# Kernel optimization log

Hardware: AMD Instinct MI355X
Metric: run time of the kernel (lower is better)

Reference implementation:

```python
import jax, jax.numpy as jnp
import numpy as np

D = 288
H = 8
HD = D // H  # 36
LAYER_TYPES = ['attn' if i % 3 == 0 else 'rec' for i in range(1, 15)]  # 4 attn, 10 rec


def rmsnorm(x, scale, eps=1e-6):
    # matches torch: ||x||_2 / sqrt(d), then scale * x / (norm + eps)
    norm = jnp.linalg.norm(x, axis=-1, keepdims=True) * (x.shape[-1] ** -0.5)
    return scale * x / (norm + eps)


def attention(x, w_qkv, w_out, nscale):
    B, L, Dm = x.shape
    r = x
    x = rmsnorm(x, nscale)
    qkv = x @ w_qkv.T  # [B,L,3D]
    q, k, v = jnp.split(qkv, 3, axis=-1)
    sh = lambda t: t.reshape(B, L, H, HD).transpose(0, 2, 1, 3)  # [B,H,L,hd]
    q, k, v = sh(q), sh(k), sh(v)
    scores = jnp.einsum('bhqd,bhkd->bhqk', q, k) / jnp.sqrt(jnp.float32(HD))
    mask = jnp.tril(jnp.ones((L, L), dtype=bool))
    scores = jnp.where(mask, scores, -jnp.inf)
    p = jax.nn.softmax(scores, axis=-1)
    o = jnp.einsum('bhqk,bhkd->bhqd', p, v).transpose(0, 2, 1, 3).reshape(B, L, Dm)
    return r + o @ w_out.T


def recurrence(x, w_in, w_out, nscale):
    r = x
    x = rmsnorm(x, nscale)
    gvf = x @ w_in.T  # [B,L,3D]
    g, v, f = jnp.split(gvf, 3, axis=-1)
    g = jax.nn.sigmoid(g)
    f = jax.nn.sigmoid(f - 1.0)
    B, L, Dm = v.shape

    def step(h, fv):
        ft, vt = fv
        h = ft * h + (1.0 - ft) * vt
        return h, h

    _, hs = jax.lax.scan(step, jnp.zeros((B, Dm), v.dtype),
                         (f.transpose(1, 0, 2), v.transpose(1, 0, 2)))
    h_seq = hs.transpose(1, 0, 2)  # [B,L,D]
    return r + (g * h_seq) @ w_out.T


def ffn(x, wg, wu, wd, nscale):
    r = x
    x = rmsnorm(x, nscale)
    return r + (jax.nn.silu(x @ wg.T) * (x @ wu.T)) @ wd.T


def setup_inputs() -> dict:
    key = jax.random.key(0)
    ks = jax.random.split(key, 16)
    n = lambda k, shape, std=0.02: jax.random.normal(k, shape, jnp.float32) * std
    return dict(
        x=jax.random.randint(ks[0], (32, 512), 0, 4096),
        emb=n(ks[1], (4096, 288)),
        pos_emb=n(ks[2], (512, 288), 0.01),
        attn_qkv=n(ks[3], (4, 864, 288)),
        attn_out=n(ks[4], (4, 288, 288)),
        attn_norm=jnp.ones((4, 288), jnp.float32),
        rec_in=n(ks[5], (10, 864, 288)),
        rec_out=n(ks[6], (10, 288, 288)),
        rec_norm=jnp.ones((10, 288), jnp.float32),
        ffn_gate=n(ks[7], (14, 864, 288)),
        ffn_up=n(ks[8], (14, 864, 288)),
        ffn_down=n(ks[9], (14, 288, 864)),
        ffn_norm=jnp.ones((14, 288), jnp.float32),
        final_norm=jnp.ones((288,), jnp.float32),
    )


def reference(x, emb, pos_emb, attn_qkv, attn_out, attn_norm,
              rec_in, rec_out, rec_norm,
              ffn_gate, ffn_up, ffn_down, ffn_norm, final_norm):
    L = x.shape[1]
    h = emb[x] + pos_emb[jnp.arange(L)]
    ai = ri = 0
    for i, t in enumerate(LAYER_TYPES):
        if t == 'attn':
            h = attention(h, attn_qkv[ai], attn_out[ai], attn_norm[ai])
            ai += 1
        else:
            h = recurrence(h, rec_in[ri], rec_out[ri], rec_norm[ri])
            ri += 1
        h = ffn(h, ffn_gate[i], ffn_up[i], ffn_down[i], ffn_norm[i])
    h = rmsnorm(h, final_norm)
    return h @ emb.T  # [B,L,V] tied-embedding logits
```

## Files before the change

kernel.cpp:

```cpp
#include <hip/hip_runtime.h>
#include <hip/hip_bf16.h>
#include <math.h>
#include <stdint.h>

using bf16 = __hip_bfloat16;
typedef __attribute__((ext_vector_type(8))) short short8;
typedef __attribute__((ext_vector_type(4))) float f32x4;

#define LOG2E 1.44269504088896340736f

enum { EPI_BF16 = 0, EPI_GVF = 1, EPI_F32 = 3 };

__device__ __forceinline__ float bf2f(bf16 v) { return __bfloat162float(v); }
__device__ __forceinline__ bf16 f2bf(float v) { return __float2bfloat16(v); }
__device__ __forceinline__ unsigned short f2bfraw(float f) {
  bf16 h = __float2bfloat16(f);
  unsigned short u;
  __builtin_memcpy(&u, &h, 2);
  return u;
}
__device__ __forceinline__ float braw2f(unsigned short u) {
  unsigned x = (unsigned)u << 16;
  float f;
  __builtin_memcpy(&f, &x, 4);
  return f;
}

__device__ __forceinline__ int swz64(int row, int col) {
  return row * 32 + ((((col >> 3) ^ ((row >> 1) & 3)) << 3) | (col & 7));
}
__device__ __forceinline__ int swz128(int row, int col) {
  return row * 64 + ((((col >> 3) ^ (row & 7)) << 3) | (col & 7));
}

__device__ __forceinline__ void gload16(const bf16* src, bf16* dst) {
  __builtin_amdgcn_global_load_lds(
      (const __attribute__((address_space(1))) void*)src,
      (__attribute__((address_space(3))) void*)dst, 16, 0, 0);
}

__global__ void cvt_kernel(const float* __restrict__ in, bf16* __restrict__ out, int n4) {
  int i = blockIdx.x * 256 + threadIdx.x;
  if (i >= n4) return;
  const float4 v = ((const float4*)in)[i];
  uint2 pk;
  pk.x = (unsigned)f2bfraw(v.x) | ((unsigned)f2bfraw(v.y) << 16);
  pk.y = (unsigned)f2bfraw(v.z) | ((unsigned)f2bfraw(v.w) << 16);
  ((uint2*)out)[i] = pk;
}

__global__ __launch_bounds__(256) void embed_norm_kernel(const int* __restrict__ x,
                                                         const float* __restrict__ emb,
                                                         const float* __restrict__ pos,
                                                         const float* __restrict__ sc,
                                                         float* __restrict__ hbuf,
                                                         bf16* __restrict__ xn) {
  int row = blockIdx.x * 4 + (threadIdx.x >> 6);
  int lane = threadIdx.x & 63;
  int tok = x[row];
  const float* e = emb + (size_t)tok * 288;
  const float* p = pos + (size_t)(row & 511) * 288;
  float v[5];
  float ss = 0.f;
#pragma unroll
  for (int j = 0; j < 4; ++j) {
    v[j] = e[j * 64 + lane] + p[j * 64 + lane];
    ss += v[j] * v[j];
  }
  v[4] = (lane < 32) ? (e[256 + lane] + p[256 + lane]) : 0.f;
  ss += v[4] * v[4];
#pragma unroll
  for (int off = 32; off > 0; off >>= 1) ss += __shfl_xor(ss, off);
  float inv = 1.f / (sqrtf(ss * (1.f / 288.f)) + 1e-6f);
  float* hr = hbuf + (size_t)row * 288;
  bf16* xr = xn + (size_t)row * 288;
#pragma unroll
  for (int j = 0; j < 4; ++j) {
    hr[j * 64 + lane] = v[j];
    xr[j * 64 + lane] = f2bf(v[j] * inv * sc[j * 64 + lane]);
  }
  if (lane < 32) {
    hr[256 + lane] = v[4];
    xr[256 + lane] = f2bf(v[4] * inv * sc[256 + lane]);
  }
}

__global__ __launch_bounds__(64) void scanA_kernel(const bf16* __restrict__ gvf,
                                                   float* __restrict__ Ap,
                                                   float* __restrict__ Bp) {
  int g = blockIdx.x * 64 + threadIdx.x;
  int c = blockIdx.y;
  int b = g / 144, dp = g - b * 144;
  const bf16* base = gvf + (size_t)b * 512 * 864 + (size_t)c * 32 * 864 + dp * 2;
  float A0 = 1.f, A1 = 1.f, B0 = 0.f, B1 = 0.f;
#pragma unroll 4
  for (int t = 0; t < 32; ++t) {
    unsigned vv = *(const unsigned*)(base + (size_t)t * 864 + 288);
    unsigned ff = *(const unsigned*)(base + (size_t)t * 864 + 576);
    float v0 = braw2f((unsigned short)vv), v1 = braw2f((unsigned short)(vv >> 16));
    float f0 = braw2f((unsigned short)ff), f1 = braw2f((unsigned short)(ff >> 16));
    B0 = f0 * B0 + (1.f - f0) * v0;
    B1 = f1 * B1 + (1.f - f1) * v1;
    A0 *= f0;
    A1 *= f1;
  }
  int half = b * 144 + dp;
  ((float2*)(Ap + (size_t)c * 9216))[half] = make_float2(A0, A1);
  ((float2*)(Bp + (size_t)c * 9216))[half] = make_float2(B0, B1);
}

__global__ __launch_bounds__(64) void scanC_kernel(const bf16* __restrict__ gvf,
                                                   const float* __restrict__ Ap,
                                                   const float* __restrict__ Bp,
                                                   bf16* __restrict__ y) {
  int g = blockIdx.x * 64 + threadIdx.x;
  int c = blockIdx.y;
  int b = g / 144, dp = g - b * 144;
  int half = b * 144 + dp;
  float h0 = 0.f, h1 = 0.f;
  for (int cc = 0; cc < c; ++cc) {
    float2 a = ((const float2*)(Ap + (size_t)cc * 9216))[half];
    float2 bb = ((const float2*)(Bp + (size_t)cc * 9216))[half];
    h0 = bb.x + a.x * h0;
    h1 = bb.y + a.y * h1;
  }
  const bf16* base = gvf + (size_t)b * 512 * 864 + (size_t)c * 32 * 864 + dp * 2;
  bf16* yb = y + (size_t)b * 512 * 288 + (size_t)c * 32 * 288 + dp * 2;
#pragma unroll 4
  for (int t = 0; t < 32; ++t) {
    unsigned gg = *(const unsigned*)(base + (size_t)t * 864);
    unsigned vv = *(const unsigned*)(base + (size_t)t * 864 + 288);
    unsigned ff = *(const unsigned*)(base + (size_t)t * 864 + 576);
    float g0 = braw2f((unsigned short)gg), g1 = braw2f((unsigned short)(gg >> 16));
    float v0 = braw2f((unsigned short)vv), v1 = braw2f((unsigned short)(vv >> 16));
    float f0 = braw2f((unsigned short)ff), f1 = braw2f((unsigned short)(ff >> 16));
    h0 = f0 * h0 + (1.f - f0) * v0;
    h1 = f1 * h1 + (1.f - f1) * v1;
    unsigned o = (unsigned)f2bfraw(g0 * h0) | ((unsigned)f2bfraw(g1 * h1) << 16);
    *(unsigned*)(yb + (size_t)t * 288) = o;
  }
}

template <int BN, int EPI>
__global__ __launch_bounds__(256) void gemm_kernel(const bf16* __restrict__ A,
                                                   const bf16* __restrict__ W,
                                                   void* __restrict__ outv,
                                                   int N, int K) {
  constexpr int WN = BN / 2;
  constexpr int NF = WN / 16;
  constexpr int TC = 8 + BN / 16;
  __shared__ __align__(16) bf16 As[2][128 * 32];
  __shared__ __align__(16) bf16 Bs[2][BN * 32];
  const int tid = threadIdx.x;
  const int w = tid >> 6, l = tid & 63;
  const int m0 = blockIdx.x * 128;
  const int n0 = blockIdx.y * BN;
  const int nk = K >> 5;
  const int lrow = l >> 2, lslot = l & 3;

  auto stage = [&](int buf, int kt) {
    for (int wc = w; wc < TC; wc += 4) {
      const bf16* src;
      bf16* dst;
      int row;
      if (wc < 8) {
        row = wc * 16 + lrow;
        src = A + (size_t)(m0 + row) * K;
        dst = &As[buf][wc * 512];
      } else {
        row = (wc - 8) * 16 + lrow;
        src = W + (size_t)(n0 + row) * K;
        dst = &Bs[buf][(wc - 8) * 512];
      }
      int slot = lslot ^ ((row >> 1) & 3);
      gload16(src + kt * 32 + slot * 8, dst);
    }
  };

  f32x4 acc[4][NF];
#pragma unroll
  for (int a = 0; a < 4; ++a)
#pragma unroll
    for (int b = 0; b < NF; ++b) acc[a][b] = (f32x4){0.f, 0.f, 0.f, 0.f};

  stage(0, 0);
  __syncthreads();
  for (int kt = 0; kt < nk; ++kt) {
    int cur = kt & 1;
    if (kt + 1 < nk) stage(cur ^ 1, kt + 1);
    short8 af[4], bfr[NF];
#pragma unroll
    for (int mf = 0; mf < 4; ++mf)
      af[mf] = *(const short8*)&As[cur][swz64((w >> 1) * 64 + mf * 16 + (l & 15), (l >> 4) * 8)];
#pragma unroll
    for (int nf = 0; nf < NF; ++nf)
      bfr[nf] = *(const short8*)&Bs[cur][swz64((w & 1) * WN + nf * 16 + (l & 15), (l >> 4) * 8)];
#pragma unroll
    for (int mf = 0; mf < 4; ++mf)
#pragma unroll
      for (int nf = 0; nf < NF; ++nf)
        acc[mf][nf] = __builtin_amdgcn_mfma_f32_16x16x32_bf16(af[mf], bfr[nf], acc[mf][nf], 0, 0, 0);
    __syncthreads();
  }

#pragma unroll
  for (int mf = 0; mf < 4; ++mf) {
#pragma unroll
    for (int nf = 0; nf < NF; ++nf) {
#pragma unroll
      for (int rr = 0; rr < 4; ++rr) {
        int row = m0 + (w >> 1) * 64 + mf * 16 + (l >> 4) * 4 + rr;
        int col = n0 + (w & 1) * WN + nf * 16 + (l & 15);
        float v = acc[mf][nf][rr];
        size_t o = (size_t)row * N + col;
        if (EPI == EPI_BF16) {
          ((bf16*)outv)[o] = f2bf(v);
        } else if (EPI == EPI_GVF) {
          float z;
          if (col < 288) z = 1.f / (1.f + __expf(-v));
          else if (col < 576) z = v;
          else z = 1.f / (1.f + __expf(-(v - 1.f)));
          ((bf16*)outv)[o] = f2bf(z);
        } else {
          ((float*)outv)[o] = v;
        }
      }
    }
  }
}

__global__ __launch_bounds__(256) void gemm_row_kernel(const bf16* __restrict__ A,
                                                       const bf16* __restrict__ W,
                                                       float* __restrict__ hbuf,
                                                       bf16* __restrict__ xn,
                                                       const float* __restrict__ scale,
                                                       int K) {
  __shared__ __align__(16) bf16 As[2][64 * 32];
  __shared__ __align__(16) bf16 Bs[2][288 * 32];
  __shared__ float ssx[2][64];
  const int tid = threadIdx.x;
  const int w = tid >> 6, l = tid & 63;
  const int m0 = blockIdx.x * 64;
  const int nk = K >> 5;
  const int lrow = l >> 2, lslot = l & 3;

  auto stage = [&](int buf, int kt) {
    for (int wc = w; wc < 22; wc += 4) {
      const bf16* src;
      bf16* dst;
      int row;
      if (wc < 4) {
        row = wc * 16 + lrow;
        src = A + (size_t)(m0 + row) * K;
        dst = &As[buf][wc * 512];
      } else {
        row = (wc - 4) * 16 + lrow;
        src = W + (size_t)row * K;
        dst = &Bs[buf][(wc - 4) * 512];
      }
      int slot = lslot ^ ((row >> 1) & 3);
      gload16(src + kt * 32 + slot * 8, dst);
    }
  };

  f32x4 acc[2][9];
#pragma unroll
  for (int a = 0; a < 2; ++a)
#pragma unroll
    for (int b = 0; b < 9; ++b) acc[a][b] = (f32x4){0.f, 0.f, 0.f, 0.f};

  stage(0, 0);
  __syncthreads();
  for (int kt = 0; kt < nk; ++kt) {
    int cur = kt & 1;
    if (kt + 1 < nk) stage(cur ^ 1, kt + 1);
    short8 af[2];
#pragma unroll
    for (int mf = 0; mf < 2; ++mf)
      af[mf] = *(const short8*)&As[cur][swz64((w >> 1) * 32 + mf * 16 + (l & 15), (l >> 4) * 8)];
#pragma unroll
    for (int nf = 0; nf < 9; ++nf) {
      short8 bv = *(const short8*)&Bs[cur][swz64((w & 1) * 144 + nf * 16 + (l & 15), (l >> 4) * 8)];
      acc[0][nf] = __builtin_amdgcn_mfma_f32_16x16x32_bf16(af[0], bv, acc[0][nf], 0, 0, 0);
      acc[1][nf] = __builtin_amdgcn_mfma_f32_16x16x32_bf16(af[1], bv, acc[1][nf], 0, 0, 0);
    }
    __syncthreads();
  }

  float ss[2][4];
#pragma unroll
  for (int mf = 0; mf < 2; ++mf)
#pragma unroll
    for (int rr = 0; rr < 4; ++rr) ss[mf][rr] = 0.f;

#pragma unroll
  for (int mf = 0; mf < 2; ++mf)
#pragma unroll
    for (int nf = 0; nf < 9; ++nf)
#pragma unroll
      for (int rr = 0; rr < 4; ++rr) {
        int rowl = (w >> 1) * 32 + mf * 16 + (l >> 4) * 4 + rr;
        int col = (w & 1) * 144 + nf * 16 + (l & 15);
        size_t o = (size_t)(m0 + rowl) * 288 + col;
        float v = acc[mf][nf][rr] + hbuf[o];
        hbuf[o] = v;
        acc[mf][nf][rr] = v;
        ss[mf][rr] += v * v;
      }
#pragma unroll
  for (int off = 1; off < 16; off <<= 1)
#pragma unroll
    for (int mf = 0; mf < 2; ++mf)
#pragma unroll
      for (int rr = 0; rr < 4; ++rr) ss[mf][rr] += __shfl_xor(ss[mf][rr], off);
  if ((l & 15) == 0) {
#pragma unroll
    for (int mf = 0; mf < 2; ++mf)
#pragma unroll
      for (int rr = 0; rr < 4; ++rr)
        ssx[w & 1][(w >> 1) * 32 + mf * 16 + (l >> 4) * 4 + rr] = ss[mf][rr];
  }
  __syncthreads();
  float inv[2][4];
#pragma unroll
  for (int mf = 0; mf < 2; ++mf)
#pragma unroll
    for (int rr = 0; rr < 4; ++rr) {
      int rowl = (w >> 1) * 32 + mf * 16 + (l >> 4) * 4 + rr;
      float tot = ssx[0][rowl] + ssx[1][rowl];
      inv[mf][rr] = 1.f / (sqrtf(tot * (1.f / 288.f)) + 1e-6f);
    }
#pragma unroll
  for (int nf = 0; nf < 9; ++nf) {
    int col = (w & 1) * 144 + nf * 16 + (l & 15);
    float sc = scale[col];
#pragma unroll
    for (int mf = 0; mf < 2; ++mf)
#pragma unroll
      for (int rr = 0; rr < 4; ++rr) {
        int rowl = (w >> 1) * 32 + mf * 16 + (l >> 4) * 4 + rr;
        size_t o = (size_t)(m0 + rowl) * 288 + col;
        xn[o] = f2bf(acc[mf][nf][rr] * inv[mf][rr] * sc);
      }
  }
}

__global__ __launch_bounds__(256) void gateup_kernel(const bf16* __restrict__ A,
                                                     const bf16* __restrict__ Wg,
                                                     const bf16* __restrict__ Wu,
                                                     bf16* __restrict__ out, int N, int K) {
  constexpr int WN = 48, NF = 3;
  __shared__ __align__(16) bf16 As[2][128 * 32];
  __shared__ __align__(16) bf16 Bg[2][96 * 32];
  __shared__ __align__(16) bf16 Bu[2][96 * 32];
  const int tid = threadIdx.x;
  const int w = tid >> 6, l = tid & 63;
  const int m0 = blockIdx.x * 128;
  const int n0 = blockIdx.y * 96;
  const int nk = K >> 5;
  const int lrow = l >> 2, lslot = l & 3;

  auto stage = [&](int buf, int kt) {
    for (int wc = w; wc < 20; wc += 4) {
      const bf16* src;
      bf16* dst;
      int row;
      if (wc < 8) {
        row = wc * 16 + lrow;
        src = A + (size_t)(m0 + row) * K;
        dst = &As[buf][wc * 512];
      } else if (wc < 14) {
        row = (wc - 8) * 16 + lrow;
        src = Wg + (size_t)(n0 + row) * K;
        dst = &Bg[buf][(wc - 8) * 512];
      } else {
        row = (wc - 14) * 16 + lrow;
        src = Wu + (size_t)(n0 + row) * K;
        dst = &Bu[buf][(wc - 14) * 512];
      }
      int slot = lslot ^ ((row >> 1) & 3);
      gload16(src + kt * 32 + slot * 8, dst);
    }
  };

  f32x4 accg[4][NF], accu[4][NF];
#pragma unroll
  for (int a = 0; a < 4; ++a)
#pragma unroll
    for (int b = 0; b < NF; ++b) {
      accg[a][b] = (f32x4){0.f, 0.f, 0.f, 0.f};
      accu[a][b] = (f32x4){0.f, 0.f, 0.f, 0.f};
    }

  stage(0, 0);
  __syncthreads();
  for (int kt = 0; kt < nk; ++kt) {
    int cur = kt & 1;
    if (kt + 1 < nk) stage(cur ^ 1, kt + 1);
    short8 af[4], bg[NF], bu[NF];
#pragma unroll
    for (int mf = 0; mf < 4; ++mf)
      af[mf] = *(const short8*)&As[cur][swz64((w >> 1) * 64 + mf * 16 + (l & 15), (l >> 4) * 8)];
#pragma unroll
    for (int nf = 0; nf < NF; ++nf) {
      bg[nf] = *(const short8*)&Bg[cur][swz64((w & 1) * WN + nf * 16 + (l & 15), (l >> 4) * 8)];
      bu[nf] = *(const short8*)&Bu[cur][swz64((w & 1) * WN + nf * 16 + (l & 15), (l >> 4) * 8)];
    }
#pragma unroll
    for (int mf = 0; mf < 4; ++mf)
#pragma unroll
      for (int nf = 0; nf < NF; ++nf) {
        accg[mf][nf] = __builtin_amdgcn_mfma_f32_16x16x32_bf16(af[mf], bg[nf], accg[mf][nf], 0, 0, 0);
        accu[mf][nf] = __builtin_amdgcn_mfma_f32_16x16x32_bf16(af[mf], bu[nf], accu[mf][nf], 0, 0, 0);
      }
    __syncthreads();
  }

#pragma unroll
  for (int mf = 0; mf < 4; ++mf)
#pragma unroll
    for (int nf = 0; nf < NF; ++nf)
#pragma unroll
      for (int rr = 0; rr < 4; ++rr) {
        int row = m0 + (w >> 1) * 64 + mf * 16 + (l >> 4) * 4 + rr;
        int col = n0 + (w & 1) * WN + nf * 16 + (l & 15);
        float g = accg[mf][nf][rr], u = accu[mf][nf][rr];
        float s = g / (1.f + __expf(-g));
        out[(size_t)row * N + col] = f2bf(s * u);
      }
}

__global__ __launch_bounds__(256) void attn_kernel(const bf16* __restrict__ qkv,
                                                   bf16* __restrict__ y) {
  const int bid = blockIdx.x;
  const int qb = bid & 7, hh = (bid >> 3) & 7, b = bid >> 6;
  const int tid = threadIdx.x, w = tid >> 6, l = tid & 63;
  __shared__ __align__(16) bf16 Qs[64 * 64];
  __shared__ __align__(16) bf16 Ks[64 * 64];
  __shared__ __align__(16) bf16 Vt[48 * 64];
  __shared__ __align__(16) bf16 Ps[64 * 64];
  const size_t bbase = (size_t)b * 512 * 864;

  for (int idx = tid; idx < 64 * 64; idx += 256) {
    ((unsigned short*)Qs)[idx] = 0;
    ((unsigned short*)Ks)[idx] = 0;
  }
  for (int idx = tid; idx < 48 * 64; idx += 256) ((unsigned short*)Vt)[idx] = 0;

  const bf16* qp = qkv + bbase + (size_t)(qb * 64) * 864 + hh * 36;
  for (int idx = tid; idx < 64 * 36; idx += 256) {
    int row = idx / 36, c = idx - row * 36;
    Qs[swz128(row, c)] = qp[(size_t)row * 864 + c];
  }
  __syncthreads();

  f32x4 oacc[3];
#pragma unroll
  for (int f = 0; f < 3; ++f) oacc[f] = (f32x4){0.f, 0.f, 0.f, 0.f};
  float mprev[4] = {-1e30f, -1e30f, -1e30f, -1e30f};
  float lsum[4] = {0.f, 0.f, 0.f, 0.f};
  const int qrow_base = qb * 64 + w * 16;

  for (int kt = 0; kt <= qb; ++kt) {
    const bf16* kp = qkv + bbase + (size_t)(kt * 64) * 864 + 288 + hh * 36;
    const bf16* vp = qkv + bbase + (size_t)(kt * 64) * 864 + 576 + hh * 36;
    for (int idx = tid; idx < 64 * 36; idx += 256) {
      int row = idx / 36, c = idx - row * 36;
      Ks[swz128(row, c)] = kp[(size_t)row * 864 + c];
      Vt[swz128(c, row)] = vp[(size_t)row * 864 + c];
    }
    __syncthreads();

    f32x4 sacc[4];
#pragma unroll
    for (int n = 0; n < 4; ++n) sacc[n] = (f32x4){0.f, 0.f, 0.f, 0.f};
#pragma unroll
    for (int s = 0; s < 2; ++s) {
      short8 aq = *(const short8*)&Qs[swz128(w * 16 + (l & 15), s * 32 + (l >> 4) * 8)];
#pragma unroll
      for (int n = 0; n < 4; ++n) {
        short8 bk = *(const short8*)&Ks[swz128(n * 16 + (l & 15), s * 32 + (l >> 4) * 8)];
        sacc[n] = __builtin_amdgcn_mfma_f32_16x16x32_bf16(aq, bk, sacc[n], 0, 0, 0);
      }
    }

    const bool diag = (kt == qb);
    float mt[4];
#pragma unroll
    for (int rr = 0; rr < 4; ++rr) {
      int qg = qrow_base + (l >> 4) * 4 + rr;
      float mx = -1e30f;
#pragma unroll
      for (int n = 0; n < 4; ++n) {
        float sv = sacc[n][rr] * (1.f / 6.f);
        if (diag) {
          int kg = kt * 64 + n * 16 + (l & 15);
          if (kg > qg) sv = -1e30f;
        }
        sacc[n][rr] = sv;
        mx = fmaxf(mx, sv);
      }
      mt[rr] = mx;
    }
#pragma unroll
    for (int off = 1; off < 16; off <<= 1)
#pragma unroll
      for (int rr = 0; rr < 4; ++rr) mt[rr] = fmaxf(mt[rr], __shfl_xor(mt[rr], off));

    float alpha[4], rs[4];
#pragma unroll
    for (int rr = 0; rr < 4; ++rr) {
      float mn = fmaxf(mprev[rr], mt[rr]);
      alpha[rr] = exp2f((mprev[rr] - mn) * LOG2E);
      mprev[rr] = mn;
      float ps = 0.f;
#pragma unroll
      for (int n = 0; n < 4; ++n) {
        float p = exp2f((sacc[n][rr] - mn) * LOG2E);
        sacc[n][rr] = p;
        ps += p;
      }
      rs[rr] = ps;
    }
#pragma unroll
    for (int off = 1; off < 16; off <<= 1)
#pragma unroll
      for (int rr = 0; rr < 4; ++rr) rs[rr] += __shfl_xor(rs[rr], off);
#pragma unroll
    for (int rr = 0; rr < 4; ++rr) lsum[rr] = lsum[rr] * alpha[rr] + rs[rr];
#pragma unroll
    for (int f = 0; f < 3; ++f)
#pragma unroll
      for (int rr = 0; rr < 4; ++rr) oacc[f][rr] *= alpha[rr];

#pragma unroll
    for (int n = 0; n < 4; ++n)
#pragma unroll
      for (int rr = 0; rr < 4; ++rr)
        Ps[swz128(w * 16 + (l >> 4) * 4 + rr, n * 16 + (l & 15))] = f2bf(sacc[n][rr]);
    __syncthreads();

#pragma unroll
    for (int s = 0; s < 2; ++s) {
      short8 ap = *(const short8*)&Ps[swz128(w * 16 + (l & 15), s * 32 + (l >> 4) * 8)];
#pragma unroll
      for (int f = 0; f < 3; ++f) {
        short8 bv = *(const short8*)&Vt[swz128(f * 16 + (l & 15), s * 32 + (l >> 4) * 8)];
        oacc[f] = __builtin_amdgcn_mfma_f32_16x16x32_bf16(ap, bv, oacc[f], 0, 0, 0);
      }
    }
    __syncthreads();
  }

#pragma unroll
  for (int rr = 0; rr < 4; ++rr) {
    float inv = 1.f / lsum[rr];
    int row = b * 512 + qb * 64 + w * 16 + (l >> 4) * 4 + rr;
    bf16* yr = y + (size_t)row * 288 + hh * 36;
#pragma unroll
    for (int f = 0; f < 3; ++f) {
      int col = f * 16 + (l & 15);
      if (col < 36) yr[col] = f2bf(oacc[f][rr] * inv);
    }
  }
}

extern "C" void kernel_launch(void* const* d_in, const int* in_sizes, int n_in,
                              void* d_out, int out_size, void* d_ws, size_t ws_size,
                              hipStream_t stream) {
  (void)in_sizes; (void)n_in; (void)out_size; (void)ws_size;
  const int* x = (const int*)d_in[0];
  const float* emb = (const float*)d_in[1];
  const float* pos = (const float*)d_in[2];
  const float* aqkv = (const float*)d_in[3];
  const float* aout = (const float*)d_in[4];
  const float* anorm = (const float*)d_in[5];
  const float* rin = (const float*)d_in[6];
  const float* rout = (const float*)d_in[7];
  const float* rnorm = (const float*)d_in[8];
  const float* fgate = (const float*)d_in[9];
  const float* fup = (const float*)d_in[10];
  const float* fdown = (const float*)d_in[11];
  const float* fnorm = (const float*)d_in[12];
  const float* finalnorm = (const float*)d_in[13];

  char* ws = (char*)d_ws;
  size_t off = 0;
  auto alloc = [&](size_t bytes) -> char* {
    char* p = ws + off;
    off += (bytes + 255) & ~(size_t)255;
    return p;
  };
  bf16* wqkv = (bf16*)alloc(4ull * 864 * 288 * 2);
  bf16* wao = (bf16*)alloc(4ull * 288 * 288 * 2);
  bf16* wrin = (bf16*)alloc(10ull * 864 * 288 * 2);
  bf16* wrout = (bf16*)alloc(10ull * 288 * 288 * 2);
  bf16* wg = (bf16*)alloc(14ull * 864 * 288 * 2);
  bf16* wu = (bf16*)alloc(14ull * 864 * 288 * 2);
  bf16* wd = (bf16*)alloc(14ull * 288 * 864 * 2);
  bf16* wemb = (bf16*)alloc(4096ull * 288 * 2);
  float* hbuf = (float*)alloc(16384ull * 288 * 4);
  bf16* xn = (bf16*)alloc(16384ull * 288 * 2);
  bf16* gvf = (bf16*)alloc(16384ull * 864 * 2);
  bf16* ybuf = (bf16*)alloc(16384ull * 288 * 2);
  float* Ap = (float*)alloc(16ull * 9216 * 4);
  float* Bp = (float*)alloc(16ull * 9216 * 4);

  auto cvt = [&](const float* src, bf16* dst, size_t n) {
    int n4 = (int)(n / 4);
    cvt_kernel<<<(n4 + 255) / 256, 256, 0, stream>>>(src, dst, n4);
  };
  cvt(aqkv, wqkv, 4ull * 864 * 288);
  cvt(aout, wao, 4ull * 288 * 288);
  cvt(rin, wrin, 10ull * 864 * 288);
  cvt(rout, wrout, 10ull * 288 * 288);
  cvt(fgate, wg, 14ull * 864 * 288);
  cvt(fup, wu, 14ull * 864 * 288);
  cvt(fdown, wd, 14ull * 288 * 864);
  cvt(emb, wemb, 4096ull * 288);

  const float* lnorm[15];
  {
    int a2 = 0, r2 = 0;
    for (int j = 0; j < 14; ++j) {
      if ((j + 1) % 3 == 0) lnorm[j] = anorm + (a2++) * 288;
      else lnorm[j] = rnorm + (r2++) * 288;
    }
    lnorm[14] = finalnorm;
  }

  embed_norm_kernel<<<4096, 256, 0, stream>>>(x, emb, pos, lnorm[0], hbuf, xn);

  int ai = 0, ri = 0;
  for (int i = 0; i < 14; ++i) {
    const bool isattn = ((i + 1) % 3 == 0);
    if (isattn) {
      gemm_kernel<96, EPI_BF16><<<dim3(128, 9), 256, 0, stream>>>(
          xn, wqkv + (size_t)ai * 864 * 288, gvf, 864, 288);
      attn_kernel<<<2048, 256, 0, stream>>>(gvf, ybuf);
      gemm_row_kernel<<<256, 256, 0, stream>>>(
          ybuf, wao + (size_t)ai * 288 * 288, hbuf, xn, fnorm + i * 288, 288);
      ++ai;
    } else {
      gemm_kernel<96, EPI_GVF><<<dim3(128, 9), 256, 0, stream>>>(
          xn, wrin + (size_t)ri * 864 * 288, gvf, 864, 288);
      scanA_kernel<<<dim3(72, 16), 64, 0, stream>>>(gvf, Ap, Bp);
      scanC_kernel<<<dim3(72, 16), 64, 0, stream>>>(gvf, Ap, Bp, ybuf);
      gemm_row_kernel<<<256, 256, 0, stream>>>(
          ybuf, wrout + (size_t)ri * 288 * 288, hbuf, xn, fnorm + i * 288, 288);
      ++ri;
    }
    gateup_kernel<<<dim3(128, 9), 256, 0, stream>>>(
        xn, wg + (size_t)i * 864 * 288, wu + (size_t)i * 864 * 288, gvf, 864, 288);
    gemm_row_kernel<<<256, 256, 0, stream>>>(
        gvf, wd + (size_t)i * 288 * 864, hbuf, xn, lnorm[i + 1], 864);
  }
  gemm_kernel<128, EPI_F32><<<dim3(128, 32), 256, 0, stream>>>(
      xn, wemb, d_out, 4096, 288);
}
```

Baseline: 2.646 ms.

## Fuse recurrence scan chunk-reduction into input GEMM, merge weight casts, widen row GEMM

The recurrence input GEMM now tiles output columns so that each block holds matching g, v and f channels. In its epilogue it computes the per-32-step chunk carry products (A, B) with lane shuffles, which removes the separate scanA pass that re-read gvf. The eight weight conversion launches become one kernel that selects source and destination by index range. The row-wise residual+norm GEMM goes to 512 threads, with each wave owning 16 rows, to raise occupancy. The trade-offs are a heavier GEMM epilogue with scattered stores, and fewer accumulators per wave in the row GEMM.

```diff
diff --git a/kernel.cpp b/kernel.cpp
--- a/kernel.cpp
+++ b/kernel.cpp
@@ -9,7 +9,7 @@
 
 #define LOG2E 1.44269504088896340736f
 
-enum { EPI_BF16 = 0, EPI_GVF = 1, EPI_F32 = 3 };
+enum { EPI_BF16 = 0, EPI_F32 = 3 };
 
 __device__ __forceinline__ float bf2f(bf16 v) { return __bfloat162float(v); }
 __device__ __forceinline__ bf16 f2bf(float v) { return __float2bfloat16(v); }
@@ -39,14 +39,28 @@
       (__attribute__((address_space(3))) void*)dst, 16, 0, 0);
 }
 
-__global__ void cvt_kernel(const float* __restrict__ in, bf16* __restrict__ out, int n4) {
+struct CvtPtrs {
+  const float* s[8];
+  bf16* d[8];
+};
+__global__ __launch_bounds__(256) void cvt_all_kernel(CvtPtrs p) {
   int i = blockIdx.x * 256 + threadIdx.x;
-  if (i >= n4) return;
-  const float4 v = ((const float4*)in)[i];
+  const float* src;
+  bf16* dst;
+  int li = i;
+  if (i < 248832)       { src = p.s[0]; dst = p.d[0]; }
+  else if (i < 331776)  { src = p.s[1]; dst = p.d[1]; li = i - 248832; }
+  else if (i < 953856)  { src = p.s[2]; dst = p.d[2]; li = i - 331776; }
+  else if (i < 1161216) { src = p.s[3]; dst = p.d[3]; li = i - 953856; }
+  else if (i < 2032128) { src = p.s[4]; dst = p.d[4]; li = i - 1161216; }
+  else if (i < 2903040) { src = p.s[5]; dst = p.d[5]; li = i - 2032128; }
+  else if (i < 3773952) { src = p.s[6]; dst = p.d[6]; li = i - 2903040; }
+  else                  { src = p.s[7]; dst = p.d[7]; li = i - 3773952; }
+  const float4 v = ((const float4*)src)[li];
   uint2 pk;
   pk.x = (unsigned)f2bfraw(v.x) | ((unsigned)f2bfraw(v.y) << 16);
   pk.y = (unsigned)f2bfraw(v.z) | ((unsigned)f2bfraw(v.w) << 16);
-  ((uint2*)out)[i] = pk;
+  ((uint2*)dst)[li] = pk;
 }
 
 __global__ __launch_bounds__(256) void embed_norm_kernel(const int* __restrict__ x,
@@ -83,30 +97,6 @@
     hr[256 + lane] = v[4];
     xr[256 + lane] = f2bf(v[4] * inv * sc[256 + lane]);
   }
-}
-
-__global__ __launch_bounds__(64) void scanA_kernel(const bf16* __restrict__ gvf,
-                                                   float* __restrict__ Ap,
-                                                   float* __restrict__ Bp) {
-  int g = blockIdx.x * 64 + threadIdx.x;
-  int c = blockIdx.y;
-  int b = g / 144, dp = g - b * 144;
-  const bf16* base = gvf + (size_t)b * 512 * 864 + (size_t)c * 32 * 864 + dp * 2;
-  float A0 = 1.f, A1 = 1.f, B0 = 0.f, B1 = 0.f;
-#pragma unroll 4
-  for (int t = 0; t < 32; ++t) {
-    unsigned vv = *(const unsigned*)(base + (size_t)t * 864 + 288);
-    unsigned ff = *(const unsigned*)(base + (size_t)t * 864 + 576);
-    float v0 = braw2f((unsigned short)vv), v1 = braw2f((unsigned short)(vv >> 16));
-    float f0 = braw2f((unsigned short)ff), f1 = braw2f((unsigned short)(ff >> 16));
-    B0 = f0 * B0 + (1.f - f0) * v0;
-    B1 = f1 * B1 + (1.f - f1) * v1;
-    A0 *= f0;
-    A1 *= f1;
-  }
-  int half = b * 144 + dp;
-  ((float2*)(Ap + (size_t)c * 9216))[half] = make_float2(A0, A1);
-  ((float2*)(Bp + (size_t)c * 9216))[half] = make_float2(B0, B1);
 }
 
 __global__ __launch_bounds__(64) void scanC_kernel(const bf16* __restrict__ gvf,
@@ -215,12 +205,6 @@
         size_t o = (size_t)row * N + col;
         if (EPI == EPI_BF16) {
           ((bf16*)outv)[o] = f2bf(v);
-        } else if (EPI == EPI_GVF) {
-          float z;
-          if (col < 288) z = 1.f / (1.f + __expf(-v));
-          else if (col < 576) z = v;
-          else z = 1.f / (1.f + __expf(-(v - 1.f)));
-          ((bf16*)outv)[o] = f2bf(z);
         } else {
           ((float*)outv)[o] = v;
         }
@@ -229,7 +213,125 @@
   }
 }
 
-__global__ __launch_bounds__(256) void gemm_row_kernel(const bf16* __restrict__ A,
+__global__ __launch_bounds__(256) void gemm_gvf_scan_kernel(const bf16* __restrict__ A,
+                                                            const bf16* __restrict__ W,
+                                                            bf16* __restrict__ gvf,
+                                                            float* __restrict__ Ap,
+                                                            float* __restrict__ Bp,
+                                                            int K) {
+  __shared__ __align__(16) bf16 As[2][128 * 32];
+  __shared__ __align__(16) bf16 Bs[2][96 * 32];
+  const int tid = threadIdx.x;
+  const int w = tid >> 6, l = tid & 63;
+  const int m0 = blockIdx.x * 128;
+  const int ch0 = blockIdx.y * 32;
+  const int nk = K >> 5;
+  const int lrow = l >> 2, lslot = l & 3;
+
+  auto stage = [&](int buf, int kt) {
+    for (int wc = w; wc < 14; wc += 4) {
+      const bf16* src;
+      bf16* dst;
+      int ldsrow;
+      if (wc < 8) {
+        ldsrow = wc * 16 + lrow;
+        src = A + (size_t)(m0 + ldsrow) * K;
+        dst = &As[buf][wc * 512];
+      } else {
+        int r96 = (wc - 8) * 16 + lrow;
+        ldsrow = r96;
+        int gr = r96 >> 4;
+        int sec = (gr >= 3) ? (gr - 3) : gr;
+        int offc = (gr >= 3) ? 16 : 0;
+        src = W + (size_t)(sec * 288 + ch0 + offc + (r96 & 15)) * K;
+        dst = &Bs[buf][(wc - 8) * 512];
+      }
+      int slot = lslot ^ ((ldsrow >> 1) & 3);
+      gload16(src + kt * 32 + slot * 8, dst);
+    }
+  };
+
+  f32x4 acc[4][3];
+#pragma unroll
+  for (int a = 0; a < 4; ++a)
+#pragma unroll
+    for (int b = 0; b < 3; ++b) acc[a][b] = (f32x4){0.f, 0.f, 0.f, 0.f};
+
+  stage(0, 0);
+  __syncthreads();
+  for (int kt = 0; kt < nk; ++kt) {
+    int cur = kt & 1;
+    if (kt + 1 < nk) stage(cur ^ 1, kt + 1);
+    short8 af[4], bfr[3];
+#pragma unroll
+    for (int mf = 0; mf < 4; ++mf)
+      af[mf] = *(const short8*)&As[cur][swz64((w >> 1) * 64 + mf * 16 + (l & 15), (l >> 4) * 8)];
+#pragma unroll
+    for (int nf = 0; nf < 3; ++nf)
+      bfr[nf] = *(const short8*)&Bs[cur][swz64((w & 1) * 48 + nf * 16 + (l & 15), (l >> 4) * 8)];
+#pragma unroll
+    for (int mf = 0; mf < 4; ++mf)
+#pragma unroll
+      for (int nf = 0; nf < 3; ++nf)
+        acc[mf][nf] = __builtin_amdgcn_mfma_f32_16x16x32_bf16(af[mf], bfr[nf], acc[mf][nf], 0, 0, 0);
+    __syncthreads();
+  }
+
+  const int chg = ch0 + (w & 1) * 16 + (l & 15);
+  const int bb = m0 >> 9;
+  const int lq = l >> 4;
+  float Asub[4], Bsub[4];
+#pragma unroll
+  for (int mf = 0; mf < 4; ++mf) {
+    float Aa = 1.f, Bb = 0.f;
+#pragma unroll
+    for (int rr = 0; rr < 4; ++rr) {
+      int row = m0 + (w >> 1) * 64 + mf * 16 + lq * 4 + rr;
+      float gv = acc[mf][0][rr];
+      float vv = acc[mf][1][rr];
+      float fv = acc[mf][2][rr];
+      float gs = 1.f / (1.f + __expf(-gv));
+      float fs = 1.f / (1.f + __expf(-(fv - 1.f)));
+      bf16 gb = f2bf(gs), vb = f2bf(vv), fb = f2bf(fs);
+      bf16* gp = gvf + (size_t)row * 864;
+      gp[chg] = gb;
+      gp[288 + chg] = vb;
+      gp[576 + chg] = fb;
+      float fr = bf2f(fb), vr = bf2f(vb);
+      Aa = fr * Aa;
+      Bb = fr * Bb + (1.f - fr) * vr;
+    }
+    Asub[mf] = Aa;
+    Bsub[mf] = Bb;
+  }
+#pragma unroll
+  for (int mf = 0; mf < 4; ++mf) {
+#pragma unroll
+    for (int bit = 16; bit <= 32; bit <<= 1) {
+      float Ao = __shfl_xor(Asub[mf], bit);
+      float Bo = __shfl_xor(Bsub[mf], bit);
+      if (l & bit) {
+        Bsub[mf] = Asub[mf] * Bo + Bsub[mf];
+        Asub[mf] = Asub[mf] * Ao;
+      } else {
+        Bsub[mf] = Ao * Bsub[mf] + Bo;
+        Asub[mf] = Ao * Asub[mf];
+      }
+    }
+  }
+  if (lq == 0) {
+    float Ac0 = Asub[1] * Asub[0], Bc0 = Asub[1] * Bsub[0] + Bsub[1];
+    float Ac1 = Asub[3] * Asub[2], Bc1 = Asub[3] * Bsub[2] + Bsub[3];
+    int cbase = ((m0 & 511) >> 5) + (w >> 1) * 2;
+    size_t ix = (size_t)bb * 288 + chg;
+    Ap[(size_t)cbase * 9216 + ix] = Ac0;
+    Bp[(size_t)cbase * 9216 + ix] = Bc0;
+    Ap[(size_t)(cbase + 1) * 9216 + ix] = Ac1;
+    Bp[(size_t)(cbase + 1) * 9216 + ix] = Bc1;
+  }
+}
+
+__global__ __launch_bounds__(512) void gemm_row_kernel(const bf16* __restrict__ A,
                                                        const bf16* __restrict__ W,
                                                        float* __restrict__ hbuf,
                                                        bf16* __restrict__ xn,
@@ -240,12 +342,13 @@
   __shared__ float ssx[2][64];
   const int tid = threadIdx.x;
   const int w = tid >> 6, l = tid & 63;
+  const int wm = w >> 1, wn = w & 1;
   const int m0 = blockIdx.x * 64;
   const int nk = K >> 5;
   const int lrow = l >> 2, lslot = l & 3;
 
   auto stage = [&](int buf, int kt) {
-    for (int wc = w; wc < 22; wc += 4) {
+    for (int wc = w; wc < 22; wc += 8) {
       const bf16* src;
       bf16* dst;
       int row;
@@ -263,85 +366,63 @@
     }
   };
 
-  f32x4 acc[2][9];
-#pragma unroll
-  for (int a = 0; a < 2; ++a)
-#pragma unroll
-    for (int b = 0; b < 9; ++b) acc[a][b] = (f32x4){0.f, 0.f, 0.f, 0.f};
+  f32x4 acc[9];
+#pragma unroll
+  for (int b = 0; b < 9; ++b) acc[b] = (f32x4){0.f, 0.f, 0.f, 0.f};
 
   stage(0, 0);
   __syncthreads();
   for (int kt = 0; kt < nk; ++kt) {
     int cur = kt & 1;
     if (kt + 1 < nk) stage(cur ^ 1, kt + 1);
-    short8 af[2];
-#pragma unroll
-    for (int mf = 0; mf < 2; ++mf)
-      af[mf] = *(const short8*)&As[cur][swz64((w >> 1) * 32 + mf * 16 + (l & 15), (l >> 4) * 8)];
+    short8 af = *(const short8*)&As[cur][swz64(wm * 16 + (l & 15), (l >> 4) * 8)];
 #pragma unroll
     for (int nf = 0; nf < 9; ++nf) {
-      short8 bv = *(const short8*)&Bs[cur][swz64((w & 1) * 144 + nf * 16 + (l & 15), (l >> 4) * 8)];
-      acc[0][nf] = __builtin_amdgcn_mfma_f32_16x16x32_bf16(af[0], bv, acc[0][nf], 0, 0, 0);
-      acc[1][nf] = __builtin_amdgcn_mfma_f32_16x16x32_bf16(af[1], bv, acc[1][nf], 0, 0, 0);
+      short8 bv = *(const short8*)&Bs[cur][swz64(wn * 144 + nf * 16 + (l & 15), (l >> 4) * 8)];
+      acc[nf] = __builtin_amdgcn_mfma_f32_16x16x32_bf16(af, bv, acc[nf], 0, 0, 0);
     }
     __syncthreads();
   }
 
-  float ss[2][4];
-#pragma unroll
-  for (int mf = 0; mf < 2; ++mf)
-#pragma unroll
-    for (int rr = 0; rr < 4; ++rr) ss[mf][rr] = 0.f;
-
-#pragma unroll
-  for (int mf = 0; mf < 2; ++mf)
-#pragma unroll
-    for (int nf = 0; nf < 9; ++nf)
-#pragma unroll
-      for (int rr = 0; rr < 4; ++rr) {
-        int rowl = (w >> 1) * 32 + mf * 16 + (l >> 4) * 4 + rr;
-        int col = (w & 1) * 144 + nf * 16 + (l & 15);
-        size_t o = (size_t)(m0 + rowl) * 288 + col;
-        float v = acc[mf][nf][rr] + hbuf[o];
-        hbuf[o] = v;
-        acc[mf][nf][rr] = v;
-        ss[mf][rr] += v * v;
-      }
+  float ss4[4] = {0.f, 0.f, 0.f, 0.f};
+#pragma unroll
+  for (int nf = 0; nf < 9; ++nf)
+#pragma unroll
+    for (int rr = 0; rr < 4; ++rr) {
+      int rowl = wm * 16 + (l >> 4) * 4 + rr;
+      int col = wn * 144 + nf * 16 + (l & 15);
+      size_t o = (size_t)(m0 + rowl) * 288 + col;
+      float v = acc[nf][rr] + hbuf[o];
+      hbuf[o] = v;
+      acc[nf][rr] = v;
+      ss4[rr] += v * v;
+    }
 #pragma unroll
   for (int off = 1; off < 16; off <<= 1)
 #pragma unroll
-    for (int mf = 0; mf < 2; ++mf)
-#pragma unroll
-      for (int rr = 0; rr < 4; ++rr) ss[mf][rr] += __shfl_xor(ss[mf][rr], off);
+    for (int rr = 0; rr < 4; ++rr) ss4[rr] += __shfl_xor(ss4[rr], off);
   if ((l & 15) == 0) {
 #pragma unroll
-    for (int mf = 0; mf < 2; ++mf)
-#pragma unroll
-      for (int rr = 0; rr < 4; ++rr)
-        ssx[w & 1][(w >> 1) * 32 + mf * 16 + (l >> 4) * 4 + rr] = ss[mf][rr];
+    for (int rr = 0; rr < 4; ++rr) ssx[wn][wm * 16 + (l >> 4) * 4 + rr] = ss4[rr];
   }
   __syncthreads();
-  float inv[2][4];
-#pragma unroll
-  for (int mf = 0; mf < 2; ++mf)
+  float inv[4];
+#pragma unroll
+  for (int rr = 0; rr < 4; ++rr) {
+    int rowl = wm * 16 + (l >> 4) * 4 + rr;
+    float tot = ssx[0][rowl] + ssx[1][rowl];
+    inv[rr] = 1.f / (sqrtf(tot * (1.f / 288.f)) + 1e-6f);
+  }
+#pragma unroll
+  for (int nf = 0; nf < 9; ++nf) {
+    int col = wn * 144 + nf * 16 + (l & 15);
+    float sc = scale[col];
 #pragma unroll
     for (int rr = 0; rr < 4; ++rr) {
-      int rowl = (w >> 1) * 32 + mf * 16 + (l >> 4) * 4 + rr;
-      float tot = ssx[0][rowl] + ssx[1][rowl];
-      inv[mf][rr] = 1.f / (sqrtf(tot * (1.f / 288.f)) + 1e-6f);
-    }
-#pragma unroll
-  for (int nf = 0; nf < 9; ++nf) {
-    int col = (w & 1) * 144 + nf * 16 + (l & 15);
-    float sc = scale[col];
-#pragma unroll
-    for (int mf = 0; mf < 2; ++mf)
-#pragma unroll
-      for (int rr = 0; rr < 4; ++rr) {
-        int rowl = (w >> 1) * 32 + mf * 16 + (l >> 4) * 4 + rr;
-        size_t o = (size_t)(m0 + rowl) * 288 + col;
-        xn[o] = f2bf(acc[mf][nf][rr] * inv[mf][rr] * sc);
-      }
+      int rowl = wm * 16 + (l >> 4) * 4 + rr;
+      size_t o = (size_t)(m0 + rowl) * 288 + col;
+      xn[o] = f2bf(acc[nf][rr] * inv[rr] * sc);
+    }
   }
 }
 
@@ -606,18 +687,16 @@
   float* Ap = (float*)alloc(16ull * 9216 * 4);
   float* Bp = (float*)alloc(16ull * 9216 * 4);
 
-  auto cvt = [&](const float* src, bf16* dst, size_t n) {
-    int n4 = (int)(n / 4);
-    cvt_kernel<<<(n4 + 255) / 256, 256, 0, stream>>>(src, dst, n4);
-  };
-  cvt(aqkv, wqkv, 4ull * 864 * 288);
-  cvt(aout, wao, 4ull * 288 * 288);
-  cvt(rin, wrin, 10ull * 864 * 288);
-  cvt(rout, wrout, 10ull * 288 * 288);
-  cvt(fgate, wg, 14ull * 864 * 288);
-  cvt(fup, wu, 14ull * 864 * 288);
-  cvt(fdown, wd, 14ull * 288 * 864);
-  cvt(emb, wemb, 4096ull * 288);
+  CvtPtrs cp;
+  cp.s[0] = aqkv;  cp.d[0] = wqkv;
+  cp.s[1] = aout;  cp.d[1] = wao;
+  cp.s[2] = rin;   cp.d[2] = wrin;
+  cp.s[3] = rout;  cp.d[3] = wrout;
+  cp.s[4] = fgate; cp.d[4] = wg;
+  cp.s[5] = fup;   cp.d[5] = wu;
+  cp.s[6] = fdown; cp.d[6] = wd;
+  cp.s[7] = emb;   cp.d[7] = wemb;
+  cvt_all_kernel<<<15894, 256, 0, stream>>>(cp);
 
   const float* lnorm[15];
   {
@@ -638,21 +717,20 @@
       gemm_kernel<96, EPI_BF16><<<dim3(128, 9), 256, 0, stream>>>(
           xn, wqkv + (size_t)ai * 864 * 288, gvf, 864, 288);
       attn_kernel<<<2048, 256, 0, stream>>>(gvf, ybuf);
-      gemm_row_kernel<<<256, 256, 0, stream>>>(
+      gemm_row_kernel<<<256, 512, 0, stream>>>(
           ybuf, wao + (size_t)ai * 288 * 288, hbuf, xn, fnorm + i * 288, 288);
       ++ai;
     } else {
-      gemm_kernel<96, EPI_GVF><<<dim3(128, 9), 256, 0, stream>>>(
-          xn, wrin + (size_t)ri * 864 * 288, gvf, 864, 288);
-      scanA_kernel<<<dim3(72, 16), 64, 0, stream>>>(gvf, Ap, Bp);
+      gemm_gvf_scan_kernel<<<dim3(128, 9), 256, 0, stream>>>(
+          xn, wrin + (size_t)ri * 864 * 288, gvf, Ap, Bp, 288);
       scanC_kernel<<<dim3(72, 16), 64, 0, stream>>>(gvf, Ap, Bp, ybuf);
-      gemm_row_kernel<<<256, 256, 0, stream>>>(
+      gemm_row_kernel<<<256, 512, 0, stream>>>(
           ybuf, wrout + (size_t)ri * 288 * 288, hbuf, xn, fnorm + i * 288, 288);
       ++ri;
     }
     gateup_kernel<<<dim3(128, 9), 256, 0, stream>>>(
         xn, wg + (size_t)i * 864 * 288, wu + (size_t)i * 864 * 288, gvf, 864, 288);
-    gemm_row_kernel<<<256, 256, 0, stream>>>(
+    gemm_row_kernel<<<256, 512, 0, stream>>>(
         gvf, wd + (size_t)i * 288 * 864, hbuf, xn, lnorm[i + 1], 864);
   }
   gemm_kernel<128, EPI_F32><<<dim3(128, 32), 256, 0, stream>>>(
```

New measurement: 2.432 ms. 8.1% less time.
